# Kernel optimization log

Hardware: AMD Instinct MI355X
Metric: run time of the kernel (lower is better)

The kernel has to match this reference:

```python
import jax, jax.numpy as jnp
import numpy as np

E, H = 1024, 16
B, N = 4, 2048
D = E // H

def setup_inputs() -> dict:
    key = jax.random.key(0)
    ks = jax.random.split(key, 5)
    s = 1.0 / np.sqrt(E)
    return {
        "x": jax.random.normal(ks[0], (B, N, E), dtype=jnp.float32),
        "Wqkv": jax.random.normal(ks[1], (E, 3 * E), dtype=jnp.float32) * s,
        "bqkv": jnp.zeros((3 * E,), dtype=jnp.float32),
        "Wproj": jax.random.normal(ks[2], (E, E), dtype=jnp.float32) * s,
        "bproj": jnp.zeros((E,), dtype=jnp.float32),
    }

def reference(x, Wqkv, bqkv, Wproj, bproj):
    b, n, e = x.shape
    qkv = x @ Wqkv + bqkv  # [b, n, 3e]
    # torch rearrange 'b n (h d qkv) -> qkv b h n d': last dim splits as (h, d, 3)
    qkv = qkv.reshape(b, n, H, D, 3)
    qkv = jnp.transpose(qkv, (4, 0, 2, 1, 3))  # [3, b, h, n, d]
    q, k, v = qkv[0], qkv[1], qkv[2]
    # NOTE: module scales by 1/sqrt(e) (full embed dim), faithfully reproduced
    att = jax.nn.softmax(jnp.einsum('bhqd,bhkd->bhqk', q, k) / jnp.sqrt(jnp.float32(E)), axis=-1)
    out = jnp.einsum('bhqk,bhkd->bhqd', att, v)  # dropout is identity in eval
    out = jnp.transpose(out, (0, 2, 1, 3)).reshape(b, n, e)  # 'b h n d -> b n (h d)'
    return out @ Wproj + bproj
```

## Files before the change

kernel.cpp:

```cpp
#include <hip/hip_runtime.h>
#include <stdint.h>

typedef unsigned short u16;
typedef __attribute__((ext_vector_type(8))) short short8;
typedef __attribute__((ext_vector_type(4))) float f32x4;

#define LOG2E 1.44269504088896340736f
#define BB 4
#define NN 2048
#define EE 1024
#define HH 16
#define DD 64
#define MM 8192
#define C3 3072

#if __has_builtin(__builtin_amdgcn_exp2f)
#define EXP2(x) __builtin_amdgcn_exp2f(x)
#else
#define EXP2(x) exp2f(x)
#endif

__device__ __forceinline__ u16 f2bf(float f) {
  union { float f; unsigned u; } v; v.f = f;
  unsigned r = v.u + 0x7fffu + ((v.u >> 16) & 1u);
  return (u16)(r >> 16);
}

__device__ __forceinline__ unsigned pk2(float a, float b) {
  union { float f; unsigned u; } x, y; x.f = a; y.f = b;
  return ((x.u + 0x8000u) >> 16) | ((y.u + 0x8000u) & 0xffff0000u);
}

__device__ __forceinline__ void async16(const void* g, void* l) {
  __builtin_amdgcn_global_load_lds((const __attribute__((address_space(1))) void*)g,
                                   (__attribute__((address_space(3))) void*)l,
                                   16, 0, 0);
}


__global__ void cast_x_kernel(const float* __restrict__ x, u16* __restrict__ xb) {
  int i = (blockIdx.x * 256 + threadIdx.x) * 4;
  float4 v = *(const float4*)(x + i);
  u16 o0 = f2bf(v.x), o1 = f2bf(v.y), o2 = f2bf(v.z), o3 = f2bf(v.w);
  ushort4 o; o.x = o0; o.y = o1; o.z = o2; o.w = o3;
  *(ushort4*)(xb + i) = o;
}

__global__ void transpose_cast(const float* __restrict__ W, u16* __restrict__ Wt,
                               int ncols, int permute) {
  __shared__ float tile[32][33];
  const int c0 = blockIdx.x * 32, k0 = blockIdx.y * 32;
  const int tx = threadIdx.x & 31, ty = threadIdx.x >> 5;
#pragma unroll
  for (int r = 0; r < 32; r += 8)
    tile[ty + r][tx] = W[(size_t)(k0 + ty + r) * ncols + c0 + tx];
  __syncthreads();
#pragma unroll
  for (int r = 0; r < 32; r += 8) {
    int c = c0 + ty + r;
    int cp = c;
    if (permute) {
      int t = c % 3, hh = c / 192, d = (c / 3) % 64;
      cp = t * 1024 + hh * 64 + d;
    }
    Wt[(size_t)cp * EE + k0 + tx] = f2bf(tile[tx][ty + r]);
  }
}

__global__ void perm_bias(const float* __restrict__ bq, float* __restrict__ bp) {
  int c = blockIdx.x * 256 + threadIdx.x;
  if (c < C3) {
    int t = c % 3, hh = c / 192, d = (c / 3) % 64;
    bp[t * 1024 + hh * 64 + d] = bq[c];
  }
}


template <int KDIM>
__device__ __forceinline__ void gemm_core(const u16* __restrict__ A, const u16* __restrict__ Bt,
                                          int m0, int n0, u16* As, u16* Bs, f32x4 acc[4][4]) {
  const int tid = threadIdx.x;
  const int lane = tid & 63, wave = tid >> 6;
  const int q = lane >> 4, r16 = lane & 15;
  const int wrow = (wave >> 1) * 64, wcol = (wave & 1) * 64;
#pragma unroll
  for (int i = 0; i < 4; i++)
#pragma unroll
    for (int j = 0; j < 4; j++) acc[i][j] = (f32x4){0.f, 0.f, 0.f, 0.f};

  for (int k0 = 0; k0 < KDIM; k0 += 32) {
#pragma unroll
    for (int i = 0; i < 2; i++) {
      int chunk = i * 256 + tid;
      async16(A + (size_t)(m0 + (chunk >> 2)) * KDIM + k0 + (chunk & 3) * 8, &As[chunk * 8]);
      async16(Bt + (size_t)(n0 + (chunk >> 2)) * KDIM + k0 + (chunk & 3) * 8, &Bs[chunk * 8]);
    }
    __syncthreads();
    short8 af[4], bf[4];
#pragma unroll
    for (int i = 0; i < 4; i++)
      af[i] = *(const short8*)&As[(wrow + i * 16 + r16) * 32 + q * 8];
#pragma unroll
    for (int i = 0; i < 4; i++)
      bf[i] = *(const short8*)&Bs[(wcol + i * 16 + r16) * 32 + q * 8];
#pragma unroll
    for (int i = 0; i < 4; i++)
#pragma unroll
      for (int j = 0; j < 4; j++)
        acc[i][j] = __builtin_amdgcn_mfma_f32_16x16x32_bf16(af[i], bf[j], acc[i][j], 0, 0, 0);
    __syncthreads();
  }
}

__global__ __launch_bounds__(256) void gemm_qkv(const u16* __restrict__ Xb, const u16* __restrict__ Wt,
                                                const float* __restrict__ bqp, u16* __restrict__ Qb,
                                                u16* __restrict__ Kb, u16* __restrict__ Vt) {
  __shared__ __align__(16) u16 As[128 * 32];
  __shared__ __align__(16) u16 Bs[128 * 32];
  f32x4 acc[4][4];
  const int m0 = blockIdx.y * 128, n0 = blockIdx.x * 128;
  gemm_core<EE>(Xb, Wt, m0, n0, As, Bs, acc);
  const int tid = threadIdx.x, lane = tid & 63, wave = tid >> 6;
  const int q = lane >> 4, r16 = lane & 15;
  const int wrow = (wave >> 1) * 64, wcol = (wave & 1) * 64;
#pragma unroll
  for (int ci = 0; ci < 4; ci++) {
    const int cp = n0 + wcol + ci * 16 + r16;
    const float bias = bqp[cp];
    const int t = cp >> 10, hh = (cp >> 6) & 15, d = cp & 63;
#pragma unroll
    for (int ri = 0; ri < 4; ri++)
#pragma unroll
      for (int r = 0; r < 4; r++) {
        const int m = m0 + wrow + ri * 16 + q * 4 + r;
        const int b = m >> 11, n = m & 2047;
        const u16 hv = f2bf(acc[ri][ci][r] + bias);
        if (t == 0)      Qb[((size_t)(b * 16 + hh) * 2048 + n) * 64 + d] = hv;
        else if (t == 1) Kb[((size_t)(b * 16 + hh) * 2048 + n) * 64 + d] = hv;
        else             Vt[((size_t)(b * 16 + hh) * 64 + d) * 2048 + n] = hv;
      }
  }
}

__global__ __launch_bounds__(256) void gemm_proj(const u16* __restrict__ Ob, const u16* __restrict__ Wt,
                                                 const float* __restrict__ bp, float* __restrict__ out) {
  __shared__ __align__(16) u16 As[128 * 32];
  __shared__ __align__(16) u16 Bs[128 * 32];
  f32x4 acc[4][4];
  const int m0 = blockIdx.y * 128, n0 = blockIdx.x * 128;
  gemm_core<EE>(Ob, Wt, m0, n0, As, Bs, acc);
  const int tid = threadIdx.x, lane = tid & 63, wave = tid >> 6;
  const int q = lane >> 4, r16 = lane & 15;
  const int wrow = (wave >> 1) * 64, wcol = (wave & 1) * 64;
#pragma unroll
  for (int ci = 0; ci < 4; ci++) {
    const int col = n0 + wcol + ci * 16 + r16;
    const float bias = bp[col];
#pragma unroll
    for (int ri = 0; ri < 4; ri++)
#pragma unroll
      for (int r = 0; r < 4; r++) {
        const int m = m0 + wrow + ri * 16 + q * 4 + r;
        out[(size_t)m * EE + col] = acc[ri][ci][r] + bias;
      }
  }
}

__global__ __launch_bounds__(256, 3) void attn_kernel(const u16* __restrict__ Qg, const u16* __restrict__ Kg,
                                                      const u16* __restrict__ Vg, u16* __restrict__ Ob) {
  __shared__ __align__(16) u16 UQP[10240];
  __shared__ __align__(16) u16 Kd[2][4096];
  __shared__ __align__(16) u16 Vd[2][4096];
  const int tid = threadIdx.x, lane = tid & 63, wave = tid >> 6;
  const int q = lane >> 4, r16 = lane & 15;
  const int bh = blockIdx.y;
  const int q0 = blockIdx.x * 128;
  const u16* Qp = Qg + ((size_t)bh * NN + q0) * DD;
  const u16* Kp = Kg + (size_t)bh * NN * DD;
  const u16* Vp = Vg + (size_t)bh * DD * NN;
  const float cs = 0.03125f * LOG2E;

#pragma unroll
  for (int i = 0; i < 4; i++) {
    int c = i * 256 + tid;
    int ks = c >> 9, rem = c & 511, row = rem >> 2, k8 = rem & 3;
    async16(Qp + row * 64 + ks * 32 + k8 * 8, &UQP[c * 8]);
  }
#pragma unroll
  for (int i = 0; i < 2; i++) {
    int c = i * 256 + tid;
    int ks = c >> 8, rem = c & 255, row = rem >> 2, k8 = rem & 3;
    async16(Kp + row * 64 + ks * 32 + k8 * 8, &Kd[0][c * 8]);
  }
#pragma unroll
  for (int i = 0; i < 2; i++) {
    int c = i * 256 + tid;
    int ks = c >> 8, rem = c & 255, d = rem >> 2, k8 = rem & 3;
    async16(Vp + d * NN + ks * 32 + k8 * 8, &Vd[0][c * 8]);
  }
  __syncthreads();

  short8 qf[2][2];
#pragma unroll
  for (int nj = 0; nj < 2; nj++)
#pragma unroll
    for (int ks = 0; ks < 2; ks++)
      qf[nj][ks] = *(const short8*)&UQP[ks * 4096 + (wave * 32 + nj * 16 + r16) * 32 + q * 8];
  __syncthreads();

  f32x4 o[2][4];
#pragma unroll
  for (int i = 0; i < 2; i++)
#pragma unroll
    for (int j = 0; j < 4; j++) o[i][j] = (f32x4){0.f, 0.f, 0.f, 0.f};
  float lsum[2] = {0.f, 0.f};

  for (int j = 0; j < 32; j++) {
    const int buf = j & 1;
    if (j < 31) {
      const u16* Kt_ = Kp + (j + 1) * 64 * 64;
#pragma unroll
      for (int i = 0; i < 2; i++) {
        int c = i * 256 + tid;
        int ks = c >> 8, rem = c & 255, row = rem >> 2, k8 = rem & 3;
        async16(Kt_ + row * 64 + ks * 32 + k8 * 8, &Kd[buf ^ 1][c * 8]);
      }
#pragma unroll
      for (int i = 0; i < 2; i++) {
        int c = i * 256 + tid;
        int ks = c >> 8, rem = c & 255, d = rem >> 2, k8 = rem & 3;
        async16(Vp + d * NN + (j + 1) * 64 + ks * 32 + k8 * 8, &Vd[buf ^ 1][c * 8]);
      }
    }

    f32x4 st[4][2];
#pragma unroll
    for (int mi = 0; mi < 4; mi++)
#pragma unroll
      for (int nj = 0; nj < 2; nj++) st[mi][nj] = (f32x4){0.f, 0.f, 0.f, 0.f};
#pragma unroll
    for (int ks = 0; ks < 2; ks++) {
      short8 kf[4];
#pragma unroll
      for (int mi = 0; mi < 4; mi++)
        kf[mi] = *(const short8*)&Kd[buf][ks * 2048 + (mi * 16 + r16) * 32 + q * 8];
#pragma unroll
      for (int mi = 0; mi < 4; mi++)
#pragma unroll
        for (int nj = 0; nj < 2; nj++)
          st[mi][nj] = __builtin_amdgcn_mfma_f32_16x16x32_bf16(kf[mi], qf[nj][ks], st[mi][nj], 0, 0, 0);
    }

#pragma unroll
    for (int mi = 0; mi < 4; mi++)
#pragma unroll
      for (int nj = 0; nj < 2; nj++) {
        float p0 = EXP2(st[mi][nj][0] * cs);
        float p1 = EXP2(st[mi][nj][1] * cs);
        float p2 = EXP2(st[mi][nj][2] * cs);
        float p3 = EXP2(st[mi][nj][3] * cs);
        lsum[nj] += (p0 + p1) + (p2 + p3);
        uint2 w; w.x = pk2(p0, p1); w.y = pk2(p2, p3);
        const int rowp = wave * 32 + nj * 16 + r16;
        *(uint2*)&UQP[(mi >> 1) * 5120 + rowp * 40 + (mi & 1) * 16 + q * 4] = w;
      }

#pragma unroll
    for (int kp = 0; kp < 2; kp++) {
      short8 af[2], vf[4];
#pragma unroll
      for (int ri = 0; ri < 2; ri++)
        af[ri] = *(const short8*)&UQP[kp * 5120 + (wave * 32 + ri * 16 + r16) * 40 + q * 8];
#pragma unroll
      for (int ci = 0; ci < 4; ci++)
        vf[ci] = *(const short8*)&Vd[buf][kp * 2048 + (ci * 16 + r16) * 32 + q * 8];
#pragma unroll
      for (int ri = 0; ri < 2; ri++)
#pragma unroll
        for (int ci = 0; ci < 4; ci++)
          o[ri][ci] = __builtin_amdgcn_mfma_f32_16x16x32_bf16(af[ri], vf[ci], o[ri][ci], 0, 0, 0);
    }

    __syncthreads();
  }

#pragma unroll
  for (int nj = 0; nj < 2; nj++) {
    lsum[nj] += __shfl_xor(lsum[nj], 16);
    lsum[nj] += __shfl_xor(lsum[nj], 32);
  }
  __syncthreads();
  float* lws = (float*)UQP + wave * 32;
  if (q == 0) { lws[r16] = lsum[0]; lws[16 + r16] = lsum[1]; }
  float linv[2][4];
#pragma unroll
  for (int ri = 0; ri < 2; ri++)
#pragma unroll
    for (int r = 0; r < 4; r++) linv[ri][r] = 1.0f / lws[ri * 16 + q * 4 + r];

  const int b = bh >> 4, h = bh & 15;
#pragma unroll
  for (int ri = 0; ri < 2; ri++)
#pragma unroll
    for (int r = 0; r < 4; r++) {
      const int n = q0 + wave * 32 + ri * 16 + q * 4 + r;
#pragma unroll
      for (int ci = 0; ci < 4; ci++) {
        const int d = ci * 16 + r16;
        Ob[((size_t)(b * NN + n)) * EE + h * 64 + d] = f2bf(o[ri][ci][r] * linv[ri][r]);
      }
    }
}


extern "C" void kernel_launch(void* const* d_in, const int* in_sizes, int n_in,
                              void* d_out, int out_size, void* d_ws, size_t ws_size,
                              hipStream_t stream) {
  const float* x     = (const float*)d_in[0];
  const float* Wqkv  = (const float*)d_in[1];
  const float* bqkv  = (const float*)d_in[2];
  const float* Wproj = (const float*)d_in[3];
  const float* bproj = (const float*)d_in[4];
  float* out = (float*)d_out;
  char* ws = (char*)d_ws;

  u16* Xb     = (u16*)(ws);
  u16* Ob     = Xb;
  u16* Qb     = (u16*)(ws + (size_t)(16 << 20));
  u16* Kb     = (u16*)(ws + (size_t)(32 << 20));
  u16* Vt     = (u16*)(ws + (size_t)(48 << 20));
  u16* WqkvT  = (u16*)(ws + (size_t)(64 << 20));
  u16* WprojT = (u16*)(ws + (size_t)(72 << 20));
  float* bqp  = (float*)(ws + (size_t)(76 << 20));

  cast_x_kernel<<<8192, 256, 0, stream>>>(x, Xb);
  transpose_cast<<<dim3(96, 32), 256, 0, stream>>>(Wqkv, WqkvT, C3, 1);
  transpose_cast<<<dim3(32, 32), 256, 0, stream>>>(Wproj, WprojT, EE, 0);
  perm_bias<<<12, 256, 0, stream>>>(bqkv, bqp);
  gemm_qkv<<<dim3(24, 64), 256, 0, stream>>>(Xb, WqkvT, bqp, Qb, Kb, Vt);
  attn_kernel<<<dim3(16, 64), 256, 0, stream>>>(Qb, Kb, Vt, Ob);
  gemm_proj<<<dim3(8, 64), 256, 0, stream>>>(Ob, WprojT, bproj, out);
}
```

Measured before the change: 316.2 us.

## Fold softmax scale into Q, compute row sums via MFMA, remap attention blocks

```diff
diff --git a/kernel.cpp b/kernel.cpp
--- a/kernel.cpp
+++ b/kernel.cpp
@@ -6,6 +6,7 @@
 typedef __attribute__((ext_vector_type(4))) float f32x4;
 
 #define LOG2E 1.44269504088896340736f
+#define CS (0.03125f * LOG2E)
 #define BB 4
 #define NN 2048
 #define EE 1024
@@ -26,10 +27,19 @@
   return (u16)(r >> 16);
 }
 
+#if __has_builtin(__builtin_amdgcn_cvt_pk_bf16_f32)
+typedef __attribute__((ext_vector_type(2))) __bf16 bf16x2;
+__device__ __forceinline__ unsigned pk2(float a, float b) {
+  union { bf16x2 v; unsigned u; } c;
+  c.v = __builtin_amdgcn_cvt_pk_bf16_f32(a, b);
+  return c.u;
+}
+#else
 __device__ __forceinline__ unsigned pk2(float a, float b) {
   union { float f; unsigned u; } x, y; x.f = a; y.f = b;
   return ((x.u + 0x8000u) >> 16) | ((y.u + 0x8000u) & 0xffff0000u);
 }
+#endif
 
 __device__ __forceinline__ void async16(const void* g, void* l) {
   __builtin_amdgcn_global_load_lds((const __attribute__((address_space(1))) void*)g,
@@ -123,22 +133,41 @@
   const int tid = threadIdx.x, lane = tid & 63, wave = tid >> 6;
   const int q = lane >> 4, r16 = lane & 15;
   const int wrow = (wave >> 1) * 64, wcol = (wave & 1) * 64;
+  const int t = (n0 + wcol) >> 10;
+  const int b = (m0 + wrow) >> 11;
 #pragma unroll
   for (int ci = 0; ci < 4; ci++) {
     const int cp = n0 + wcol + ci * 16 + r16;
     const float bias = bqp[cp];
-    const int t = cp >> 10, hh = (cp >> 6) & 15, d = cp & 63;
-#pragma unroll
-    for (int ri = 0; ri < 4; ri++)
-#pragma unroll
-      for (int r = 0; r < 4; r++) {
-        const int m = m0 + wrow + ri * 16 + q * 4 + r;
-        const int b = m >> 11, n = m & 2047;
-        const u16 hv = f2bf(acc[ri][ci][r] + bias);
-        if (t == 0)      Qb[((size_t)(b * 16 + hh) * 2048 + n) * 64 + d] = hv;
-        else if (t == 1) Kb[((size_t)(b * 16 + hh) * 2048 + n) * 64 + d] = hv;
-        else             Vt[((size_t)(b * 16 + hh) * 64 + d) * 2048 + n] = hv;
-      }
+    const int hh = (cp >> 6) & 15, d = cp & 63;
+    if (t == 0) {
+#pragma unroll
+      for (int ri = 0; ri < 4; ri++)
+#pragma unroll
+        for (int r = 0; r < 4; r++) {
+          const int m = m0 + wrow + ri * 16 + q * 4 + r;
+          Qb[((size_t)(b * 16 + hh) * 2048 + (m & 2047)) * 64 + d] = f2bf((acc[ri][ci][r] + bias) * CS);
+        }
+    } else if (t == 1) {
+#pragma unroll
+      for (int ri = 0; ri < 4; ri++)
+#pragma unroll
+        for (int r = 0; r < 4; r++) {
+          const int m = m0 + wrow + ri * 16 + q * 4 + r;
+          Kb[((size_t)(b * 16 + hh) * 2048 + (m & 2047)) * 64 + d] = f2bf(acc[ri][ci][r] + bias);
+        }
+    } else {
+#pragma unroll
+      for (int ri = 0; ri < 4; ri++) {
+        const int nb = (m0 + wrow + ri * 16 + q * 4) & 2047;
+        ushort4 w;
+        w.x = f2bf(acc[ri][ci][0] + bias);
+        w.y = f2bf(acc[ri][ci][1] + bias);
+        w.z = f2bf(acc[ri][ci][2] + bias);
+        w.w = f2bf(acc[ri][ci][3] + bias);
+        *(ushort4*)&Vt[((size_t)(b * 16 + hh) * 64 + d) * 2048 + nb] = w;
+      }
+    }
   }
 }
 
@@ -168,24 +197,26 @@
 
 __global__ __launch_bounds__(256, 3) void attn_kernel(const u16* __restrict__ Qg, const u16* __restrict__ Kg,
                                                       const u16* __restrict__ Vg, u16* __restrict__ Ob) {
-  __shared__ __align__(16) u16 UQP[10240];
+  __shared__ __align__(16) u16 Ps[10240];
   __shared__ __align__(16) u16 Kd[2][4096];
   __shared__ __align__(16) u16 Vd[2][4096];
   const int tid = threadIdx.x, lane = tid & 63, wave = tid >> 6;
   const int q = lane >> 4, r16 = lane & 15;
-  const int bh = blockIdx.y;
-  const int q0 = blockIdx.x * 128;
+  const int id = blockIdx.x + 16 * blockIdx.y;
+  const int g = id & 7, s = id >> 3;
+  const int bh = g * 8 + (s >> 4);
+  const int q0 = (s & 15) * 128;
   const u16* Qp = Qg + ((size_t)bh * NN + q0) * DD;
   const u16* Kp = Kg + (size_t)bh * NN * DD;
   const u16* Vp = Vg + (size_t)bh * DD * NN;
-  const float cs = 0.03125f * LOG2E;
-
-#pragma unroll
-  for (int i = 0; i < 4; i++) {
-    int c = i * 256 + tid;
-    int ks = c >> 9, rem = c & 511, row = rem >> 2, k8 = rem & 3;
-    async16(Qp + row * 64 + ks * 32 + k8 * 8, &UQP[c * 8]);
-  }
+
+  short8 qf[2][2];
+#pragma unroll
+  for (int nj = 0; nj < 2; nj++)
+#pragma unroll
+    for (int ks = 0; ks < 2; ks++)
+      qf[nj][ks] = *(const short8*)(Qp + (wave * 32 + nj * 16 + r16) * 64 + ks * 32 + q * 8);
+
 #pragma unroll
   for (int i = 0; i < 2; i++) {
     int c = i * 256 + tid;
@@ -200,20 +231,16 @@
   }
   __syncthreads();
 
-  short8 qf[2][2];
-#pragma unroll
-  for (int nj = 0; nj < 2; nj++)
-#pragma unroll
-    for (int ks = 0; ks < 2; ks++)
-      qf[nj][ks] = *(const short8*)&UQP[ks * 4096 + (wave * 32 + nj * 16 + r16) * 32 + q * 8];
-  __syncthreads();
-
   f32x4 o[2][4];
-#pragma unroll
-  for (int i = 0; i < 2; i++)
+  f32x4 ol[2];
+#pragma unroll
+  for (int i = 0; i < 2; i++) {
+    ol[i] = (f32x4){0.f, 0.f, 0.f, 0.f};
 #pragma unroll
     for (int j = 0; j < 4; j++) o[i][j] = (f32x4){0.f, 0.f, 0.f, 0.f};
-  float lsum[2] = {0.f, 0.f};
+  }
+  const short8 ones = {16256, 16256, 16256, 16256, 16256, 16256, 16256, 16256};
+  u16* Pw = Ps + wave * 2560;
 
   for (int j = 0; j < 32; j++) {
     const int buf = j & 1;
@@ -255,14 +282,13 @@
     for (int mi = 0; mi < 4; mi++)
 #pragma unroll
       for (int nj = 0; nj < 2; nj++) {
-        float p0 = EXP2(st[mi][nj][0] * cs);
-        float p1 = EXP2(st[mi][nj][1] * cs);
-        float p2 = EXP2(st[mi][nj][2] * cs);
-        float p3 = EXP2(st[mi][nj][3] * cs);
-        lsum[nj] += (p0 + p1) + (p2 + p3);
+        float p0 = EXP2(st[mi][nj][0]);
+        float p1 = EXP2(st[mi][nj][1]);
+        float p2 = EXP2(st[mi][nj][2]);
+        float p3 = EXP2(st[mi][nj][3]);
         uint2 w; w.x = pk2(p0, p1); w.y = pk2(p2, p3);
-        const int rowp = wave * 32 + nj * 16 + r16;
-        *(uint2*)&UQP[(mi >> 1) * 5120 + rowp * 40 + (mi & 1) * 16 + q * 4] = w;
+        const int rowl = nj * 16 + r16;
+        *(uint2*)&Pw[(mi >> 1) * 1280 + rowl * 40 + (mi & 1) * 16 + q * 4] = w;
       }
 
 #pragma unroll
@@ -270,44 +296,33 @@
       short8 af[2], vf[4];
 #pragma unroll
       for (int ri = 0; ri < 2; ri++)
-        af[ri] = *(const short8*)&UQP[kp * 5120 + (wave * 32 + ri * 16 + r16) * 40 + q * 8];
+        af[ri] = *(const short8*)&Pw[kp * 1280 + (ri * 16 + r16) * 40 + q * 8];
 #pragma unroll
       for (int ci = 0; ci < 4; ci++)
         vf[ci] = *(const short8*)&Vd[buf][kp * 2048 + (ci * 16 + r16) * 32 + q * 8];
 #pragma unroll
-      for (int ri = 0; ri < 2; ri++)
+      for (int ri = 0; ri < 2; ri++) {
 #pragma unroll
         for (int ci = 0; ci < 4; ci++)
           o[ri][ci] = __builtin_amdgcn_mfma_f32_16x16x32_bf16(af[ri], vf[ci], o[ri][ci], 0, 0, 0);
+        ol[ri] = __builtin_amdgcn_mfma_f32_16x16x32_bf16(af[ri], ones, ol[ri], 0, 0, 0);
+      }
     }
 
     __syncthreads();
   }
 
-#pragma unroll
-  for (int nj = 0; nj < 2; nj++) {
-    lsum[nj] += __shfl_xor(lsum[nj], 16);
-    lsum[nj] += __shfl_xor(lsum[nj], 32);
-  }
-  __syncthreads();
-  float* lws = (float*)UQP + wave * 32;
-  if (q == 0) { lws[r16] = lsum[0]; lws[16 + r16] = lsum[1]; }
-  float linv[2][4];
+  const int b = bh >> 4, h = bh & 15;
 #pragma unroll
   for (int ri = 0; ri < 2; ri++)
 #pragma unroll
-    for (int r = 0; r < 4; r++) linv[ri][r] = 1.0f / lws[ri * 16 + q * 4 + r];
-
-  const int b = bh >> 4, h = bh & 15;
-#pragma unroll
-  for (int ri = 0; ri < 2; ri++)
-#pragma unroll
     for (int r = 0; r < 4; r++) {
+      const float inv = 1.0f / ol[ri][r];
       const int n = q0 + wave * 32 + ri * 16 + q * 4 + r;
 #pragma unroll
       for (int ci = 0; ci < 4; ci++) {
         const int d = ci * 16 + r16;
-        Ob[((size_t)(b * NN + n)) * EE + h * 64 + d] = f2bf(o[ri][ci][r] * linv[ri][r]);
+        Ob[((size_t)(b * NN + n)) * EE + h * 64 + d] = f2bf(o[ri][ci][r] * inv);
       }
     }
 }
```

Result: faster. 299.4 us (-5.3%).
